# Kernel tuning notes

Measured on AMD Instinct MI355X. Metric: run time of the kernel, lower is better.

Reference implementation:

```python
import jax, jax.numpy as jnp
import numpy as np
import math

B, S, D = 2, 2048, 1024
H, HD = 16, 64
ROT = 16          # rotary_dim = head_dim * 0.25
FF = 4096
EPS = 1e-5


def setup_inputs() -> dict:
    key = jax.random.key(0)
    ks = jax.random.split(key, 12)
    sc = lambda *sh: 0.02
    inp = {
        "x": jax.random.normal(ks[0], (B, S, D), jnp.float32),
        "attention_mask": jnp.tril(jnp.ones((S, S), bool))[None, None],  # causal [1,1,S,S]
        "W_qkv": jax.random.normal(ks[1], (3 * D, D), jnp.float32) * 0.02,
        "b_qkv": jnp.zeros((3 * D,), jnp.float32),
        "W_o": jax.random.normal(ks[2], (D, D), jnp.float32) * 0.02,
        "b_o": jnp.zeros((D,), jnp.float32),
        "ln1_w": jnp.ones((D,), jnp.float32),
        "ln1_b": jnp.zeros((D,), jnp.float32),
        "ln2_w": jnp.ones((D,), jnp.float32),
        "ln2_b": jnp.zeros((D,), jnp.float32),
        "W1": jax.random.normal(ks[3], (FF, D), jnp.float32) * 0.02,
        "b1": jnp.zeros((FF,), jnp.float32),
        "W2": jax.random.normal(ks[4], (D, FF), jnp.float32) * 0.02,
        "b2": jnp.zeros((D,), jnp.float32),
    }
    # real rotary frequencies, shaped [1,1,S,ROT//2,2]
    inv_freq = 1.0 / (10000.0 ** (jnp.arange(0, ROT, 2, dtype=jnp.float32) / ROT))
    t = jnp.arange(S, dtype=jnp.float32)
    ang = t[:, None] * inv_freq[None, :]                      # [S, ROT//2]
    inp["freqs_cis"] = jnp.stack([jnp.cos(ang), jnp.sin(ang)], -1)[None, None]
    return inp


def layer_norm(x, w, b):
    mu = jnp.mean(x, -1, keepdims=True)
    var = jnp.mean(jnp.square(x - mu), -1, keepdims=True)
    return (x - mu) * jax.lax.rsqrt(var + EPS) * w + b


def apply_rotate_emb(x, freqs_cis):
    # x: [B,H,S,ROT]; freqs_cis: [1,1,S,ROT//2,2]
    x1, x2 = x[..., : ROT // 2], x[..., ROT // 2 :]
    cos, sin = freqs_cis[..., 0], freqs_cis[..., 1]
    return jnp.concatenate([x1 * cos - x2 * sin, x1 * sin + x2 * cos], -1)


def reference(x, attention_mask, freqs_cis, W_qkv, b_qkv, W_o, b_o,
              ln1_w, ln1_b, ln2_w, ln2_b, W1, b1, W2, b2):
    h = layer_norm(x, ln1_w, ln1_b)
    qkv = jnp.einsum("bsd,ed->bse", h, W_qkv) + b_qkv
    q, k, v = jnp.split(qkv, 3, axis=-1)
    to_heads = lambda t: t.reshape(B, S, H, HD).transpose(0, 2, 1, 3)  # [B,H,S,HD]
    q, k, v = to_heads(q), to_heads(k), to_heads(v)
    q = jnp.concatenate([apply_rotate_emb(q[..., :ROT], freqs_cis), q[..., ROT:]], -1)
    k = jnp.concatenate([apply_rotate_emb(k[..., :ROT], freqs_cis), k[..., ROT:]], -1)
    scores = jnp.einsum("bhqd,bhkd->bhqk", q, k) / math.sqrt(HD)
    scores = jnp.where(attention_mask, scores, -jnp.inf)
    probs = jax.nn.softmax(scores, axis=-1)
    out = jnp.einsum("bhqk,bhkd->bhqd", probs, v)
    out = out.transpose(0, 2, 1, 3).reshape(B, S, D)
    attn_out = jnp.einsum("bsd,ed->bse", out, W_o) + b_o
    # parallel residual (dropout is identity in eval)
    h2 = layer_norm(x, ln2_w, ln2_b)
    ff = jnp.einsum("bsf,df->bsd", jax.nn.gelu(jnp.einsum("bsd,fd->bsf", h2, W1) + b1, approximate=False), W2) + b2
    return x + ff + attn_out
```

## Files before the change

kernel.cpp:

```cpp
#include <hip/hip_runtime.h>

#define DEV __device__ __forceinline__

typedef __bf16 bf16;
typedef bf16 bf16x4 __attribute__((ext_vector_type(4)));
typedef bf16 bf16x8 __attribute__((ext_vector_type(8)));
typedef float f32x4 __attribute__((ext_vector_type(4)));

DEV f32x4 mfma16(bf16x8 a, bf16x8 b, f32x4 c) {
  return __builtin_amdgcn_mfma_f32_16x16x32_bf16(a, b, c, 0, 0, 0);
}

DEV void gload_lds16(const bf16* g, bf16* l) {
  __builtin_amdgcn_global_load_lds((const __attribute__((address_space(1))) void*)g,
                                   (__attribute__((address_space(3))) void*)l, 16, 0, 0);
}

#define PH_BAR __builtin_amdgcn_s_barrier()
#define VM(NSTR) asm volatile("s_waitcnt vmcnt(" NSTR ")" ::: "memory")
#define VMLG(NSTR) asm volatile("s_waitcnt vmcnt(" NSTR ") lgkmcnt(0)" ::: "memory")
#define WAITBAR(NSTR) asm volatile("s_waitcnt vmcnt(" NSTR ")\n\ts_barrier" ::: "memory")

DEV float fast_gelu(float x) {
  const float z = x * x;
  const float w = __builtin_fmaf(z, 0.1029353f, 2.3019853f);
  const float e = __builtin_amdgcn_exp2f(x * w);
  const float r = __builtin_amdgcn_rcpf(1.0f + e);
  return x - x * r;
}

__global__ __launch_bounds__(256) void ln_cast_all(
    const float* __restrict__ x,
    const float* __restrict__ ln1w, const float* __restrict__ ln1b,
    const float* __restrict__ ln2w, const float* __restrict__ ln2b,
    bf16* __restrict__ h1, bf16* __restrict__ h2,
    const float* __restrict__ Wqkv_f, const float* __restrict__ W1_f,
    const float* __restrict__ Wo_f, const float* __restrict__ W2_f,
    bf16* __restrict__ wQKV, bf16* __restrict__ w1, bf16* __restrict__ wCat)
{
  const int b = blockIdx.x, t = threadIdx.x;
  if (b < 4096) {
    __shared__ float red[2][4];
    const int lane = t & 63, wave = t >> 6;
    const float4 v = ((const float4*)(x + (size_t)b * 1024))[t];
    float vv[4] = {v.x, v.y, v.z, v.w};
    float s = vv[0] + vv[1] + vv[2] + vv[3];
    float q = vv[0]*vv[0] + vv[1]*vv[1] + vv[2]*vv[2] + vv[3]*vv[3];
    #pragma unroll
    for (int o = 32; o; o >>= 1) { s += __shfl_xor(s, o); q += __shfl_xor(q, o); }
    if (lane == 0) { red[0][wave] = s; red[1][wave] = q; }
    __syncthreads();
    s = red[0][0] + red[0][1] + red[0][2] + red[0][3];
    q = red[1][0] + red[1][1] + red[1][2] + red[1][3];
    const float mu = s * (1.0f / 1024.0f);
    const float var = q * (1.0f / 1024.0f) - mu * mu;
    const float rs = rsqrtf(var + 1e-5f);
    bf16x4 o1, o2;
    #pragma unroll
    for (int j = 0; j < 4; ++j) {
      const int i = t * 4 + j;
      const float xh = (vv[j] - mu) * rs;
      o1[j] = (bf16)(xh * ln1w[i] + ln1b[i]);
      o2[j] = (bf16)(xh * ln2w[i] + ln2b[i]);
    }
    *(bf16x4*)&h1[(size_t)b * 1024 + t * 4] = o1;
    *(bf16x4*)&h2[(size_t)b * 1024 + t * 4] = o2;
    return;
  }
  const int cb = b - 4096;
  if (cb < 3072) {
    const int i = cb * 256 + t;
    const float4 v = ((const float4*)Wqkv_f)[i];
    bf16x4 o = {(bf16)v.x, (bf16)v.y, (bf16)v.z, (bf16)v.w};
    ((bf16x4*)wQKV)[i] = o;
  } else if (cb < 7168) {
    const int i = (cb - 3072) * 256 + t;
    const float4 v = ((const float4*)W1_f)[i];
    bf16x4 o = {(bf16)v.x, (bf16)v.y, (bf16)v.z, (bf16)v.w};
    ((bf16x4*)w1)[i] = o;
  } else if (cb < 8192) {
    const int row = cb - 7168;
    const float4 v = *(const float4*)&Wo_f[(size_t)row * 1024 + t * 4];
    bf16x4 o = {(bf16)v.x, (bf16)v.y, (bf16)v.z, (bf16)v.w};
    *(bf16x4*)&wCat[(size_t)row * 5120 + t * 4] = o;
  } else {
    const int row = cb - 8192;
    #pragma unroll
    for (int k = 0; k < 4; ++k) {
      const int col = t * 4 + k * 1024;
      const float4 v = *(const float4*)&W2_f[(size_t)row * 4096 + col];
      bf16x4 o = {(bf16)v.x, (bf16)v.y, (bf16)v.z, (bf16)v.w};
      *(bf16x4*)&wCat[(size_t)row * 5120 + 1024 + col] = o;
    }
  }
}

DEV bf16x8 ldfrag(const bf16* unit, int lr, int g) {
  return *(const bf16x8*)&unit[lr * 32 + ((g ^ ((lr >> 1) & 3)) << 3)];
}
DEV void read_bfr(const bf16* unit, int blr, int g, bf16x8 bfr[4]) {
  #pragma unroll
  for (int nj = 0; nj < 4; ++nj) bfr[nj] = ldfrag(unit, blr + nj * 16, g);
}
DEV void read_af(const bf16* unit, int alr, int g, bf16x8 af[4]) {
  #pragma unroll
  for (int ml = 0; ml < 4; ++ml) af[ml] = ldfrag(unit, alr + ml * 16, g);
}
DEV void do_mfma(const bf16x8 af[4], const bf16x8 bfr[4], f32x4 acc[8][4], int mh) {
  __builtin_amdgcn_s_setprio(1);
  #pragma unroll
  for (int ml = 0; ml < 4; ++ml)
    #pragma unroll
    for (int nj = 0; nj < 4; ++nj)
      acc[mh * 4 + ml][nj] = mfma16(af[ml], bfr[nj], acc[mh * 4 + ml][nj]);
  __builtin_amdgcn_s_setprio(0);
}

DEV void gemm_kloop(bf16 (*As)[2][2][4096], bf16 (*Bs)[2][2][4096],
                    const bf16* aU[2][2], const bf16* bU[2][2],
                    int wave, int alr, int blr, int bub, int g, int nkt,
                    f32x4 acc[8][4])
{
  bf16x8 bfr[4], af[4];
#define STG_A(bf_, kkh_, ub_, ko_) gload_lds16(aU[kkh_][ub_] + (ko_), &As[bf_][kkh_][ub_][wave * 512])
#define STG_B(bf_, kkh_, ub_, ko_) gload_lds16(bU[kkh_][ub_] + (ko_), &Bs[bf_][kkh_][ub_][wave * 512])
  STG_B(0, 0, 0, 0); STG_B(0, 0, 1, 0); STG_A(0, 0, 0, 0); STG_A(0, 0, 1, 0);
  STG_B(0, 1, 0, 0); STG_B(0, 1, 1, 0); STG_A(0, 1, 0, 0); STG_A(0, 1, 1, 0);
  WAITBAR("4");

  for (int t = 0; t < nkt - 1; ++t) {
    const int buf = t & 1, nxt = buf ^ 1;
    const int ko = (t + 1) * 64;
    read_bfr(&Bs[buf][0][bub][0], blr, g, bfr);
    read_af(&As[buf][0][0][0], alr, g, af);
    STG_B(nxt, 0, 0, ko); STG_B(nxt, 0, 1, ko);
    do_mfma(af, bfr, acc, 0);
    read_af(&As[buf][0][1][0], alr, g, af);
    STG_A(nxt, 0, 0, ko); STG_A(nxt, 0, 1, ko);
    do_mfma(af, bfr, acc, 1);
    VMLG("4");
    PH_BAR;
    read_bfr(&Bs[buf][1][bub][0], blr, g, bfr);
    read_af(&As[buf][1][0][0], alr, g, af);
    STG_B(nxt, 1, 0, ko); STG_B(nxt, 1, 1, ko);
    do_mfma(af, bfr, acc, 0);
    read_af(&As[buf][1][1][0], alr, g, af);
    STG_A(nxt, 1, 0, ko); STG_A(nxt, 1, 1, ko);
    do_mfma(af, bfr, acc, 1);
    VMLG("4");
    PH_BAR;
  }
  {
    const int buf = (nkt - 1) & 1;
    read_bfr(&Bs[buf][0][bub][0], blr, g, bfr);
    read_af(&As[buf][0][0][0], alr, g, af);
    do_mfma(af, bfr, acc, 0);
    read_af(&As[buf][0][1][0], alr, g, af);
    do_mfma(af, bfr, acc, 1);
    VMLG("0");
    PH_BAR;
    read_bfr(&Bs[buf][1][bub][0], blr, g, bfr);
    read_af(&As[buf][1][0][0], alr, g, af);
    do_mfma(af, bfr, acc, 0);
    read_af(&As[buf][1][1][0], alr, g, af);
    do_mfma(af, bfr, acc, 1);
  }
#undef STG_A
#undef STG_B
}

template <int EPI>
__global__ __launch_bounds__(512) void gemm256(
    const bf16* __restrict__ A, const bf16* __restrict__ B,
    const float* __restrict__ bias, void* __restrict__ Cv,
    void* __restrict__ P1, void* __restrict__ P2, void* __restrict__ P3,
    const float* __restrict__ freqs,
    int K, int ldc, int ntiles, int nbx, int nkt)
{
  __shared__ __align__(16) bf16 As[2][2][2][4096];
  __shared__ __align__(16) bf16 Bs[2][2][2][4096];
  const int tid = threadIdx.x;
  const int lane = tid & 63, wave = tid >> 6;
  const int wm = wave >> 2, wn = wave & 3;
  const int g = lane >> 4, c = lane & 15;
  const int cpx = gridDim.x >> 3;
  const int swz = ((int)blockIdx.x & 7) * cpx + ((int)blockIdx.x >> 3);
  const int tile = swz % ntiles;
  const int sk = swz / ntiles;
  const int bm = (tile / nbx) * 256, bn = (tile % nbx) * 256;

  const int slr = tid >> 2;
  const int sch = (tid & 3) ^ ((tid >> 3) & 3);
  const bf16* aU[2][2];
  const bf16* bU[2][2];
  {
    const bf16* a0 = A + (size_t)(bm + ((slr >> 6) * 128) + (slr & 63)) * K
                       + (size_t)sk * nkt * 64 + sch * 8;
    const bf16* b0 = B + (size_t)(bn + slr) * K + (size_t)sk * nkt * 64 + sch * 8;
    aU[0][0] = a0;            aU[0][1] = a0 + (size_t)64 * K;
    aU[1][0] = a0 + 32;       aU[1][1] = a0 + (size_t)64 * K + 32;
    bU[0][0] = b0;            bU[0][1] = b0 + (size_t)128 * K;
    bU[1][0] = b0 + 32;       bU[1][1] = b0 + (size_t)128 * K + 32;
  }

  f32x4 acc[8][4] = {};
  const int alr = (wm << 6) + c;
  const int blr = ((wn & 1) << 6) + c;
  const int bub = wn >> 1;

  gemm_kloop(As, Bs, aU, bU, wave, alr, blr, bub, g, nkt, acc);

  const int row0 = bm + wm * 128 + 4 * g;
  const int col0 = bn + wn * 64 + c;

  if constexpr (EPI == 3) {
    bf16* Qb  = (bf16*)Cv;
    bf16* Kb  = (bf16*)P1;
    bf16* VTb = (bf16*)P2;
    const int which = bn >> 10;
    const int h = ((bn & 1023) >> 6) + wn;
    #pragma unroll
    for (int mi = 0; mi < 8; ++mi) {
      const int srow = row0 + mi * 16;
      const int bb = srow >> 11, sl0 = srow & 2047;
      #pragma unroll
      for (int nj = 0; nj < 4; ++nj) {
        const int d = nj * 16 + c;
        const float bv = bias[bn + wn * 64 + d];
        float vo[4];
        #pragma unroll
        for (int r = 0; r < 4; ++r) vo[r] = acc[mi][nj][r] + bv;
        if (which == 2) {
          bf16x4 o = {(bf16)vo[0], (bf16)vo[1], (bf16)vo[2], (bf16)vo[3]};
          *(bf16x4*)&VTb[((size_t)(bb * 16 + h) * 64 + d) * 2048 + sl0] = o;
        } else {
          if (nj == 0) {
            #pragma unroll
            for (int r = 0; r < 4; ++r) {
              const int sl = sl0 + r;
              const float cs = freqs[sl * 16 + (c & 7) * 2];
              const float sn = freqs[sl * 16 + (c & 7) * 2 + 1];
              const float p = __shfl_xor(vo[r], 8);
              vo[r] = (c < 8) ? (vo[r] * cs - p * sn) : (p * sn + vo[r] * cs);
            }
          }
          bf16* dst = (which == 0) ? Qb : Kb;
          const float sc = (which == 0) ? 0.18033688f  : 1.0f;
          #pragma unroll
          for (int r = 0; r < 4; ++r)
            dst[((size_t)(bb * 16 + h) * 2048 + (sl0 + r)) * 64 + d] = (bf16)(vo[r] * sc);
        }
      }
    }
    return;
  }

  bf16* Pp = nullptr;
  if constexpr (EPI == 2)
    Pp = (bf16*)((sk == 1) ? P1 : (sk == 2) ? P2 : (sk == 3) ? P3 : Cv);
  #pragma unroll
  for (int mi = 0; mi < 8; ++mi) {
    #pragma unroll
    for (int nj = 0; nj < 4; ++nj) {
      const int col = col0 + nj * 16;
      float bv = 0.0f;
      if constexpr (EPI < 2) bv = bias[col];
      #pragma unroll
      for (int r = 0; r < 4; ++r) {
        const size_t idx = (size_t)(row0 + mi * 16 + r) * ldc + col;
        float vo = acc[mi][nj][r] + bv;
        if constexpr (EPI == 0) {
          ((bf16*)Cv)[idx] = (bf16)vo;
        } else if constexpr (EPI == 1) {
          ((bf16*)Cv)[idx] = (bf16)fast_gelu(vo);
        } else {
          Pp[idx] = (bf16)vo;
        }
      }
    }
  }
}

__global__ __launch_bounds__(256) void combine_out(
    const bf16* __restrict__ q0, const bf16* __restrict__ q1,
    const bf16* __restrict__ q2, const bf16* __restrict__ q3,
    const float* __restrict__ x,
    const float* __restrict__ bo, const float* __restrict__ b2,
    float* __restrict__ out)
{
  const int row = blockIdx.x, t = threadIdx.x;
  const size_t base = (size_t)row * 1024 + t * 4;
  const bf16x4 a0 = *(const bf16x4*)&q0[base];
  const bf16x4 a1 = *(const bf16x4*)&q1[base];
  const bf16x4 a2 = *(const bf16x4*)&q2[base];
  const bf16x4 a3 = *(const bf16x4*)&q3[base];
  const float4 vx = *(const float4*)&x[base];
  const float4 vb = *(const float4*)&bo[t * 4];
  const float4 vc = *(const float4*)&b2[t * 4];
  float4 o;
  o.x = (float)a0[0] + (float)a1[0] + (float)a2[0] + (float)a3[0] + vx.x + vb.x + vc.x;
  o.y = (float)a0[1] + (float)a1[1] + (float)a2[1] + (float)a3[1] + vx.y + vb.y + vc.y;
  o.z = (float)a0[2] + (float)a1[2] + (float)a2[2] + (float)a3[2] + vx.z + vb.z + vc.z;
  o.w = (float)a0[3] + (float)a1[3] + (float)a2[3] + (float)a3[3] + vx.w + vb.w + vc.w;
  *(float4*)&out[base] = o;
}

__global__ __launch_bounds__(512, 4) void attn_kernel(
    const bf16* __restrict__ Q, const bf16* __restrict__ Kg,
    const bf16* __restrict__ VTg, bf16* __restrict__ O, int ldO)
{
  __shared__ __align__(16) bf16 Ks[4][64][64];
  __shared__ __align__(16) bf16 Vs[4][64][64];
  __shared__ __align__(16) bf16 Ps[8][16][64];

  const int tid = threadIdx.x;
  const int lane = tid & 63, wave = tid >> 6;
  const int g = lane >> 4, c = lane & 15;
  const int L = blockIdx.x;
  const int heavy = (L < 256);
  const int r = heavy ? L : (L - 256);
  const int bh = r >> 3;
  const int qtile = heavy ? (8 + (r & 7)) : (7 - (r & 7));
  const int qw = qtile * 128 + wave * 16;

  const bf16* Qp = Q + (size_t)bh * 2048 * 64;
  const bf16* Kp = Kg + (size_t)bh * 2048 * 64;
  const bf16* Vp = VTg + (size_t)bh * 64 * 2048;

  const int srow = lane >> 3;
  const int schunk = (lane & 7) ^ srow;
  const int svr = wave * 8 + srow;

  bf16x8 qreg[2];
  qreg[0] = *(const bf16x8*)&Qp[(size_t)(qw + c) * 64 + g * 8];
  qreg[1] = *(const bf16x8*)&Qp[(size_t)(qw + c) * 64 + 32 + g * 8];
  bf16x8 ones;
  #pragma unroll
  for (int j = 0; j < 8; ++j) ones[j] = (bf16)1.0f;

  const int cq = c & 7;
  int fo[4][2];
  #pragma unroll
  for (int i = 0; i < 4; ++i)
    #pragma unroll
    for (int kk = 0; kk < 2; ++kk)
      fo[i][kk] = (i * 16 + c) * 64 + (((kk * 4 + g) ^ cq) << 3);
  bf16* pw[4];
  #pragma unroll
  for (int kf = 0; kf < 4; ++kf)
    pw[kf] = &Ps[wave][c][((((kf * 2 + (g >> 1)) ^ cq) << 3)) + ((g & 1) << 2)];
  const bf16* pr[2];
  #pragma unroll
  for (int kk = 0; kk < 2; ++kk)
    pr[kk] = &Ps[wave][c][((kk * 4 + g) ^ cq) << 3];

  bf16* const kdst[4] = {&Ks[0][0][0] + wave * 512, &Ks[1][0][0] + wave * 512,
                         &Ks[2][0][0] + wave * 512, &Ks[3][0][0] + wave * 512};
  bf16* const vdst[4] = {&Vs[0][0][0] + wave * 512, &Vs[1][0][0] + wave * 512,
                         &Vs[2][0][0] + wave * 512, &Vs[3][0][0] + wave * 512};

  f32x4 oacc[4] = {};
  f32x4 lacc = {};
  float m_ = -1e30f;

  const int nkb = 2 * qtile + 2;
#define STAGE(j_, B4_) do {                                                         \
    gload_lds16(&Kp[(size_t)((j_) * 64 + svr) * 64 + schunk * 8], kdst[B4_]);       \
    gload_lds16(&Vp[(size_t)svr * 2048 + (j_) * 64 + schunk * 8], vdst[B4_]);       \
  } while (0)

  auto qkt = [&](f32x4* st, const bf16* kt) {
    __builtin_amdgcn_s_setprio(1);
    #pragma unroll
    for (int kf = 0; kf < 4; ++kf) {
      f32x4 z = {};
      z = mfma16(*(const bf16x8*)(kt + fo[kf][0]), qreg[0], z);
      st[kf] = mfma16(*(const bf16x8*)(kt + fo[kf][1]), qreg[1], z);
    }
    __builtin_amdgcn_s_setprio(0);
  };

  auto smpv = [&](const f32x4* st, int j_, const bf16* vt) {
    const int kbase = j_ * 64;
    float v[16];
    if (kbase + 63 > qw) {
      const int qrel = qw + c - kbase;
      #pragma unroll
      for (int kf = 0; kf < 4; ++kf)
        #pragma unroll
        for (int rr = 0; rr < 4; ++rr)
          v[kf * 4 + rr] = (kf * 16 + 4 * g + rr <= qrel) ? st[kf][rr] : -1e30f;
    } else {
      #pragma unroll
      for (int kf = 0; kf < 4; ++kf)
        #pragma unroll
        for (int rr = 0; rr < 4; ++rr)
          v[kf * 4 + rr] = st[kf][rr];
    }
    float u0 = fmaxf(fmaxf(v[0], v[1]), v[2]);
    float u1 = fmaxf(fmaxf(v[3], v[4]), v[5]);
    float u2 = fmaxf(fmaxf(v[6], v[7]), v[8]);
    float u3 = fmaxf(fmaxf(v[9], v[10]), v[11]);
    float u4 = fmaxf(fmaxf(v[12], v[13]), v[14]);
    float tm = fmaxf(fmaxf(fmaxf(u0, u1), u2), fmaxf(fmaxf(u3, u4), v[15]));
    if (__any(tm > m_ + 8.0f)) {
      float tr = fmaxf(tm, __shfl_xor(tm, 16));
      tr = fmaxf(tr, __shfl_xor(tr, 32));
      const float mn = fmaxf(m_, tr);
      const float alpha = __builtin_amdgcn_exp2f(m_ - mn);
      m_ = mn;
      lacc[0] *= alpha; lacc[1] *= alpha; lacc[2] *= alpha; lacc[3] *= alpha;
      #pragma unroll
      for (int df = 0; df < 4; ++df) {
        oacc[df][0] *= alpha; oacc[df][1] *= alpha;
        oacc[df][2] *= alpha; oacc[df][3] *= alpha;
      }
    }
    bf16 pq[16];
    #pragma unroll
    for (int i = 0; i < 16; ++i)
      pq[i] = (bf16)__builtin_amdgcn_exp2f(v[i] - m_);
    #pragma unroll
    for (int kf = 0; kf < 4; ++kf) {
      bf16x4 pk = {pq[kf * 4], pq[kf * 4 + 1], pq[kf * 4 + 2], pq[kf * 4 + 3]};
      *(bf16x4*)pw[kf] = pk;
    }
    bf16x8 pfrag0 = *(const bf16x8*)pr[0];
    bf16x8 pfrag1 = *(const bf16x8*)pr[1];
    __builtin_amdgcn_s_setprio(1);
    #pragma unroll
    for (int df = 0; df < 4; ++df) {
      oacc[df] = mfma16(*(const bf16x8*)(vt + fo[df][0]), pfrag0, oacc[df]);
      oacc[df] = mfma16(*(const bf16x8*)(vt + fo[df][1]), pfrag1, oacc[df]);
    }
    lacc = mfma16(ones, pfrag0, lacc);
    lacc = mfma16(ones, pfrag1, lacc);
    __builtin_amdgcn_s_setprio(0);
  };

#define ABODY(j_, BUF, stC, stN) do {                                          \
    const bool stg_ = ((j_) + 3 < nkb);                                        \
    if (stg_) STAGE((j_) + 3, (((BUF) + 3) & 3));                              \
    if (((j_) + 1) < nkb && ((j_) + 1) * 64 <= qw + 15)                        \
      qkt(stN, &Ks[((BUF) + 1) & 3][0][0]);                                    \
    if ((j_) * 64 <= qw + 15) smpv(stC, (j_), &Vs[(BUF)][0][0]);               \
    if (stg_) { VM("2"); } else { VM("0"); }                                   \
    PH_BAR;                                                                    \
  } while (0)

  f32x4 stA[4], stB[4];
  STAGE(0, 0); STAGE(1, 1); STAGE(2, 2);
  VM("2");
  PH_BAR;
  qkt(stA, &Ks[0][0][0]);

  const int nq = nkb >> 2;
  for (int qd = 0; qd < nq; ++qd) {
    const int j0 = 4 * qd;
    ABODY(j0 + 0, 0, stA, stB);
    ABODY(j0 + 1, 1, stB, stA);
    ABODY(j0 + 2, 2, stA, stB);
    ABODY(j0 + 3, 3, stB, stA);
  }
  if (nkb & 2) {
    ABODY(nkb - 2, 0, stA, stB);
    ABODY(nkb - 1, 1, stB, stA);
  }
#undef ABODY
#undef STAGE

  const int b = bh >> 4, h = bh & 15;
  const float inv = 1.0f / lacc[0];
  const int s = qw + c;
  #pragma unroll
  for (int df = 0; df < 4; ++df) {
    bf16x4 o;
    #pragma unroll
    for (int rr = 0; rr < 4; ++rr) o[rr] = (bf16)(oacc[df][rr] * inv);
    *(bf16x4*)&O[(size_t)(b * 2048 + s) * ldO + h * 64 + df * 16 + 4 * g] = o;
  }
}

extern "C" void kernel_launch(void* const* d_in, const int* in_sizes, int n_in,
                              void* d_out, int out_size, void* d_ws, size_t ws_size,
                              hipStream_t stream) {
  const float* x     = (const float*)d_in[0];
  const float* W_qkv = (const float*)d_in[2];
  const float* b_qkv = (const float*)d_in[3];
  const float* W_o   = (const float*)d_in[4];
  const float* b_o   = (const float*)d_in[5];
  const float* ln1w  = (const float*)d_in[6];
  const float* ln1b  = (const float*)d_in[7];
  const float* ln2w  = (const float*)d_in[8];
  const float* ln2b  = (const float*)d_in[9];
  const float* W1    = (const float*)d_in[10];
  const float* b1    = (const float*)d_in[11];
  const float* W2    = (const float*)d_in[12];
  const float* b2    = (const float*)d_in[13];
  const float* freqs = (const float*)d_in[14];
  float* out = (float*)d_out;

  char* ws = (char*)d_ws;
  const size_t MB = (size_t)1 << 20;
  bf16* h1   = (bf16*)(ws + 0 * MB);
  bf16* h2   = (bf16*)(ws + 8 * MB);
  bf16* wQKV = (bf16*)(ws + 16 * MB);
  bf16* wCat = (bf16*)(ws + 22 * MB);
  bf16* w1   = (bf16*)(ws + 32 * MB);
  bf16* Qb   = (bf16*)(ws + 64 * MB);
  bf16* Kb   = (bf16*)(ws + 72 * MB);
  bf16* VTb  = (bf16*)(ws + 80 * MB);
  bf16* A2   = (bf16*)(ws + 88 * MB);
  bf16* q0   = (bf16*)(ws + 0 * MB);
  bf16* q1   = (bf16*)(ws + 8 * MB);
  bf16* q2   = (bf16*)(ws + 40 * MB);
  bf16* q3   = (bf16*)(ws + 48 * MB);

  ln_cast_all<<<13312, 256, 0, stream>>>(x, ln1w, ln1b, ln2w, ln2b, h1, h2,
                                         W_qkv, W1, W_o, W2, wQKV, w1, wCat);
  gemm256<3><<<192, 512, 0, stream>>>(h1, wQKV, b_qkv, Qb,
                                      Kb, VTb, nullptr, freqs,
                                      1024, 3072, 192, 12, 16);
  attn_kernel<<<512, 512, 0, stream>>>(Qb, Kb, VTb, A2, 5120);
  gemm256<1><<<256, 512, 0, stream>>>(h2, w1, b1, A2 + 1024,
                                      nullptr, nullptr, nullptr, nullptr,
                                      1024, 5120, 256, 16, 16);
  gemm256<2><<<256, 512, 0, stream>>>(A2, wCat, nullptr, q0,
                                      q1, q2, q3, nullptr,
                                      5120, 1024, 64, 4, 20);
  combine_out<<<4096, 256, 0, stream>>>(q0, q1, q2, q3, x, b_o, b2, out);
}
```

Measured before the change: 184.7 us.

## Restructure GEMM k-loop to one barrier per tile with staggered half-step order

```diff
diff --git a/kernel.cpp b/kernel.cpp
--- a/kernel.cpp
+++ b/kernel.cpp
@@ -19,7 +19,6 @@
 #define PH_BAR __builtin_amdgcn_s_barrier()
 #define VM(NSTR) asm volatile("s_waitcnt vmcnt(" NSTR ")" ::: "memory")
 #define VMLG(NSTR) asm volatile("s_waitcnt vmcnt(" NSTR ") lgkmcnt(0)" ::: "memory")
-#define WAITBAR(NSTR) asm volatile("s_waitcnt vmcnt(" NSTR ")\n\ts_barrier" ::: "memory")
 
 DEV float fast_gelu(float x) {
   const float z = x * x;
@@ -115,56 +114,59 @@
       acc[mh * 4 + ml][nj] = mfma16(af[ml], bfr[nj], acc[mh * 4 + ml][nj]);
   __builtin_amdgcn_s_setprio(0);
 }
+DEV void half_step(const bf16* bunit, const bf16* aunit0, const bf16* aunit1,
+                   int alr, int blr, int g, f32x4 acc[8][4]) {
+  bf16x8 bfr[4], af[4];
+  read_bfr(bunit, blr, g, bfr);
+  read_af(aunit0, alr, g, af);
+  do_mfma(af, bfr, acc, 0);
+  read_af(aunit1, alr, g, af);
+  do_mfma(af, bfr, acc, 1);
+}
 
 DEV void gemm_kloop(bf16 (*As)[2][2][4096], bf16 (*Bs)[2][2][4096],
                     const bf16* aU[2][2], const bf16* bU[2][2],
-                    int wave, int alr, int blr, int bub, int g, int nkt,
+                    int wave, int wm, int alr, int blr, int bub, int g, int nkt,
                     f32x4 acc[8][4])
 {
-  bf16x8 bfr[4], af[4];
 #define STG_A(bf_, kkh_, ub_, ko_) gload_lds16(aU[kkh_][ub_] + (ko_), &As[bf_][kkh_][ub_][wave * 512])
 #define STG_B(bf_, kkh_, ub_, ko_) gload_lds16(bU[kkh_][ub_] + (ko_), &Bs[bf_][kkh_][ub_][wave * 512])
-  STG_B(0, 0, 0, 0); STG_B(0, 0, 1, 0); STG_A(0, 0, 0, 0); STG_A(0, 0, 1, 0);
-  STG_B(0, 1, 0, 0); STG_B(0, 1, 1, 0); STG_A(0, 1, 0, 0); STG_A(0, 1, 1, 0);
-  WAITBAR("4");
+#define STG_TILE(bf_, ko_) do {                                                   \
+    STG_B(bf_, 0, 0, ko_); STG_B(bf_, 0, 1, ko_);                                 \
+    STG_A(bf_, 0, 0, ko_); STG_A(bf_, 0, 1, ko_);                                 \
+    STG_B(bf_, 1, 0, ko_); STG_B(bf_, 1, 1, ko_);                                 \
+    STG_A(bf_, 1, 0, ko_); STG_A(bf_, 1, 1, ko_);                                 \
+  } while (0)
+
+  STG_TILE(0, 0);
+  VMLG("0");
+  PH_BAR;
 
   for (int t = 0; t < nkt - 1; ++t) {
     const int buf = t & 1, nxt = buf ^ 1;
     const int ko = (t + 1) * 64;
-    read_bfr(&Bs[buf][0][bub][0], blr, g, bfr);
-    read_af(&As[buf][0][0][0], alr, g, af);
-    STG_B(nxt, 0, 0, ko); STG_B(nxt, 0, 1, ko);
-    do_mfma(af, bfr, acc, 0);
-    read_af(&As[buf][0][1][0], alr, g, af);
-    STG_A(nxt, 0, 0, ko); STG_A(nxt, 0, 1, ko);
-    do_mfma(af, bfr, acc, 1);
-    VMLG("4");
-    PH_BAR;
-    read_bfr(&Bs[buf][1][bub][0], blr, g, bfr);
-    read_af(&As[buf][1][0][0], alr, g, af);
-    STG_B(nxt, 1, 0, ko); STG_B(nxt, 1, 1, ko);
-    do_mfma(af, bfr, acc, 0);
-    read_af(&As[buf][1][1][0], alr, g, af);
-    STG_A(nxt, 1, 0, ko); STG_A(nxt, 1, 1, ko);
-    do_mfma(af, bfr, acc, 1);
-    VMLG("4");
+    STG_TILE(nxt, ko);
+    if (wm == 0) {
+      half_step(&Bs[buf][0][bub][0], &As[buf][0][0][0], &As[buf][0][1][0], alr, blr, g, acc);
+      half_step(&Bs[buf][1][bub][0], &As[buf][1][0][0], &As[buf][1][1][0], alr, blr, g, acc);
+    } else {
+      half_step(&Bs[buf][1][bub][0], &As[buf][1][0][0], &As[buf][1][1][0], alr, blr, g, acc);
+      half_step(&Bs[buf][0][bub][0], &As[buf][0][0][0], &As[buf][0][1][0], alr, blr, g, acc);
+    }
+    VMLG("0");
     PH_BAR;
   }
   {
     const int buf = (nkt - 1) & 1;
-    read_bfr(&Bs[buf][0][bub][0], blr, g, bfr);
-    read_af(&As[buf][0][0][0], alr, g, af);
-    do_mfma(af, bfr, acc, 0);
-    read_af(&As[buf][0][1][0], alr, g, af);
-    do_mfma(af, bfr, acc, 1);
-    VMLG("0");
-    PH_BAR;
-    read_bfr(&Bs[buf][1][bub][0], blr, g, bfr);
-    read_af(&As[buf][1][0][0], alr, g, af);
-    do_mfma(af, bfr, acc, 0);
-    read_af(&As[buf][1][1][0], alr, g, af);
-    do_mfma(af, bfr, acc, 1);
-  }
+    if (wm == 0) {
+      half_step(&Bs[buf][0][bub][0], &As[buf][0][0][0], &As[buf][0][1][0], alr, blr, g, acc);
+      half_step(&Bs[buf][1][bub][0], &As[buf][1][0][0], &As[buf][1][1][0], alr, blr, g, acc);
+    } else {
+      half_step(&Bs[buf][1][bub][0], &As[buf][1][0][0], &As[buf][1][1][0], alr, blr, g, acc);
+      half_step(&Bs[buf][0][bub][0], &As[buf][0][0][0], &As[buf][0][1][0], alr, blr, g, acc);
+    }
+  }
+#undef STG_TILE
 #undef STG_A
 #undef STG_B
 }
@@ -208,7 +210,7 @@
   const int blr = ((wn & 1) << 6) + c;
   const int bub = wn >> 1;
 
-  gemm_kloop(As, Bs, aU, bU, wave, alr, blr, bub, g, nkt, acc);
+  gemm_kloop(As, Bs, aU, bU, wave, wm, alr, blr, bub, g, nkt, acc);
 
   const int row0 = bm + wm * 128 + 4 * g;
   const int col0 = bn + wn * 64 + c;
```

After: 204.8 us. +10.9%, slower.

## Pair heavy and light causal query tiles per block, two 16-row fragments per wave

Applied to the files above, without the earlier changes.

```diff
diff --git a/kernel.cpp b/kernel.cpp
--- a/kernel.cpp
+++ b/kernel.cpp
@@ -305,23 +305,22 @@
   *(float4*)&out[base] = o;
 }
 
-__global__ __launch_bounds__(512, 4) void attn_kernel(
+__global__ __launch_bounds__(512, 2) void attn_kernel(
     const bf16* __restrict__ Q, const bf16* __restrict__ Kg,
     const bf16* __restrict__ VTg, bf16* __restrict__ O, int ldO)
 {
   __shared__ __align__(16) bf16 Ks[4][64][64];
   __shared__ __align__(16) bf16 Vs[4][64][64];
-  __shared__ __align__(16) bf16 Ps[8][16][64];
+  __shared__ __align__(16) bf16 Ps[8][2][16][64];
 
   const int tid = threadIdx.x;
   const int lane = tid & 63, wave = tid >> 6;
   const int g = lane >> 4, c = lane & 15;
   const int L = blockIdx.x;
-  const int heavy = (L < 256);
-  const int r = heavy ? L : (L - 256);
-  const int bh = r >> 3;
-  const int qtile = heavy ? (8 + (r & 7)) : (7 - (r & 7));
-  const int qw = qtile * 128 + wave * 16;
+  const int bh = L >> 3, p = L & 7;
+  const int side = wave >> 2, ws = wave & 3;
+  const int qtile = side ? (7 - p) : (8 + p);
+  const int qw = qtile * 128 + ws * 32;
 
   const bf16* Qp = Q + (size_t)bh * 2048 * 64;
   const bf16* Kp = Kg + (size_t)bh * 2048 * 64;
@@ -331,9 +330,12 @@
   const int schunk = (lane & 7) ^ srow;
   const int svr = wave * 8 + srow;
 
-  bf16x8 qreg[2];
-  qreg[0] = *(const bf16x8*)&Qp[(size_t)(qw + c) * 64 + g * 8];
-  qreg[1] = *(const bf16x8*)&Qp[(size_t)(qw + c) * 64 + 32 + g * 8];
+  bf16x8 qreg[2][2];
+  #pragma unroll
+  for (int f = 0; f < 2; ++f) {
+    qreg[f][0] = *(const bf16x8*)&Qp[(size_t)(qw + f * 16 + c) * 64 + g * 8];
+    qreg[f][1] = *(const bf16x8*)&Qp[(size_t)(qw + f * 16 + c) * 64 + 32 + g * 8];
+  }
   bf16x8 ones;
   #pragma unroll
   for (int j = 0; j < 8; ++j) ones[j] = (bf16)1.0f;
@@ -345,110 +347,149 @@
     #pragma unroll
     for (int kk = 0; kk < 2; ++kk)
       fo[i][kk] = (i * 16 + c) * 64 + (((kk * 4 + g) ^ cq) << 3);
-  bf16* pw[4];
-  #pragma unroll
-  for (int kf = 0; kf < 4; ++kf)
-    pw[kf] = &Ps[wave][c][((((kf * 2 + (g >> 1)) ^ cq) << 3)) + ((g & 1) << 2)];
-  const bf16* pr[2];
-  #pragma unroll
-  for (int kk = 0; kk < 2; ++kk)
-    pr[kk] = &Ps[wave][c][((kk * 4 + g) ^ cq) << 3];
+  bf16* pw[2][4];
+  #pragma unroll
+  for (int f = 0; f < 2; ++f)
+    #pragma unroll
+    for (int kf = 0; kf < 4; ++kf)
+      pw[f][kf] = &Ps[wave][f][c][((((kf * 2 + (g >> 1)) ^ cq) << 3)) + ((g & 1) << 2)];
+  const bf16* pr[2][2];
+  #pragma unroll
+  for (int f = 0; f < 2; ++f)
+    #pragma unroll
+    for (int kk = 0; kk < 2; ++kk)
+      pr[f][kk] = &Ps[wave][f][c][((kk * 4 + g) ^ cq) << 3];
 
   bf16* const kdst[4] = {&Ks[0][0][0] + wave * 512, &Ks[1][0][0] + wave * 512,
                          &Ks[2][0][0] + wave * 512, &Ks[3][0][0] + wave * 512};
   bf16* const vdst[4] = {&Vs[0][0][0] + wave * 512, &Vs[1][0][0] + wave * 512,
                          &Vs[2][0][0] + wave * 512, &Vs[3][0][0] + wave * 512};
 
-  f32x4 oacc[4] = {};
-  f32x4 lacc = {};
-  float m_ = -1e30f;
-
-  const int nkb = 2 * qtile + 2;
+  f32x4 oacc[2][4] = {};
+  f32x4 lacc[2] = {};
+  float m0_ = -1e30f, m1_ = -1e30f;
+
+  const int nkb = 18 + 2 * p;
 #define STAGE(j_, B4_) do {                                                         \
     gload_lds16(&Kp[(size_t)((j_) * 64 + svr) * 64 + schunk * 8], kdst[B4_]);       \
     gload_lds16(&Vp[(size_t)svr * 2048 + (j_) * 64 + schunk * 8], vdst[B4_]);       \
   } while (0)
 
-  auto qkt = [&](f32x4* st, const bf16* kt) {
+  auto qkt = [&](f32x4 (*st)[4], const bf16* kt) {
     __builtin_amdgcn_s_setprio(1);
     #pragma unroll
     for (int kf = 0; kf < 4; ++kf) {
-      f32x4 z = {};
-      z = mfma16(*(const bf16x8*)(kt + fo[kf][0]), qreg[0], z);
-      st[kf] = mfma16(*(const bf16x8*)(kt + fo[kf][1]), qreg[1], z);
+      bf16x8 k0 = *(const bf16x8*)(kt + fo[kf][0]);
+      bf16x8 k1 = *(const bf16x8*)(kt + fo[kf][1]);
+      f32x4 z0 = {}, z1 = {};
+      z0 = mfma16(k0, qreg[0][0], z0);
+      st[0][kf] = mfma16(k1, qreg[0][1], z0);
+      z1 = mfma16(k0, qreg[1][0], z1);
+      st[1][kf] = mfma16(k1, qreg[1][1], z1);
     }
     __builtin_amdgcn_s_setprio(0);
   };
 
-  auto smpv = [&](const f32x4* st, int j_, const bf16* vt) {
+  auto smpv = [&](f32x4 (*st)[4], int j_, const bf16* vt) {
     const int kbase = j_ * 64;
-    float v[16];
+    float v0[16], v1[16];
     if (kbase + 63 > qw) {
-      const int qrel = qw + c - kbase;
+      const int qr0 = qw + c - kbase;
+      const int qr1 = qr0 + 16;
       #pragma unroll
       for (int kf = 0; kf < 4; ++kf)
         #pragma unroll
-        for (int rr = 0; rr < 4; ++rr)
-          v[kf * 4 + rr] = (kf * 16 + 4 * g + rr <= qrel) ? st[kf][rr] : -1e30f;
+        for (int rr = 0; rr < 4; ++rr) {
+          const int key = kf * 16 + 4 * g + rr;
+          v0[kf * 4 + rr] = (key <= qr0) ? st[0][kf][rr] : -1e30f;
+          v1[kf * 4 + rr] = (key <= qr1) ? st[1][kf][rr] : -1e30f;
+        }
     } else {
       #pragma unroll
       for (int kf = 0; kf < 4; ++kf)
         #pragma unroll
-        for (int rr = 0; rr < 4; ++rr)
-          v[kf * 4 + rr] = st[kf][rr];
-    }
-    float u0 = fmaxf(fmaxf(v[0], v[1]), v[2]);
-    float u1 = fmaxf(fmaxf(v[3], v[4]), v[5]);
-    float u2 = fmaxf(fmaxf(v[6], v[7]), v[8]);
-    float u3 = fmaxf(fmaxf(v[9], v[10]), v[11]);
-    float u4 = fmaxf(fmaxf(v[12], v[13]), v[14]);
-    float tm = fmaxf(fmaxf(fmaxf(u0, u1), u2), fmaxf(fmaxf(u3, u4), v[15]));
-    if (__any(tm > m_ + 8.0f)) {
-      float tr = fmaxf(tm, __shfl_xor(tm, 16));
-      tr = fmaxf(tr, __shfl_xor(tr, 32));
-      const float mn = fmaxf(m_, tr);
-      const float alpha = __builtin_amdgcn_exp2f(m_ - mn);
-      m_ = mn;
-      lacc[0] *= alpha; lacc[1] *= alpha; lacc[2] *= alpha; lacc[3] *= alpha;
+        for (int rr = 0; rr < 4; ++rr) {
+          v0[kf * 4 + rr] = st[0][kf][rr];
+          v1[kf * 4 + rr] = st[1][kf][rr];
+        }
+    }
+    float t0a = fmaxf(fmaxf(v0[0], v0[1]), v0[2]);
+    float t0b = fmaxf(fmaxf(v0[3], v0[4]), v0[5]);
+    float t0c = fmaxf(fmaxf(v0[6], v0[7]), v0[8]);
+    float t0d = fmaxf(fmaxf(v0[9], v0[10]), v0[11]);
+    float t0e = fmaxf(fmaxf(v0[12], v0[13]), v0[14]);
+    float tm0 = fmaxf(fmaxf(fmaxf(t0a, t0b), t0c), fmaxf(fmaxf(t0d, t0e), v0[15]));
+    float t1a = fmaxf(fmaxf(v1[0], v1[1]), v1[2]);
+    float t1b = fmaxf(fmaxf(v1[3], v1[4]), v1[5]);
+    float t1c = fmaxf(fmaxf(v1[6], v1[7]), v1[8]);
+    float t1d = fmaxf(fmaxf(v1[9], v1[10]), v1[11]);
+    float t1e = fmaxf(fmaxf(v1[12], v1[13]), v1[14]);
+    float tm1 = fmaxf(fmaxf(fmaxf(t1a, t1b), t1c), fmaxf(fmaxf(t1d, t1e), v1[15]));
+    if (__any(fmaxf(tm0 - m0_, tm1 - m1_) > 8.0f)) {
+      float tr0 = fmaxf(tm0, __shfl_xor(tm0, 16));
+      tr0 = fmaxf(tr0, __shfl_xor(tr0, 32));
+      float tr1 = fmaxf(tm1, __shfl_xor(tm1, 16));
+      tr1 = fmaxf(tr1, __shfl_xor(tr1, 32));
+      const float mn0 = fmaxf(m0_, tr0);
+      const float mn1 = fmaxf(m1_, tr1);
+      const float a0 = __builtin_amdgcn_exp2f(m0_ - mn0);
+      const float a1 = __builtin_amdgcn_exp2f(m1_ - mn1);
+      m0_ = mn0; m1_ = mn1;
+      lacc[0][0] *= a0; lacc[0][1] *= a0; lacc[0][2] *= a0; lacc[0][3] *= a0;
+      lacc[1][0] *= a1; lacc[1][1] *= a1; lacc[1][2] *= a1; lacc[1][3] *= a1;
       #pragma unroll
       for (int df = 0; df < 4; ++df) {
-        oacc[df][0] *= alpha; oacc[df][1] *= alpha;
-        oacc[df][2] *= alpha; oacc[df][3] *= alpha;
+        oacc[0][df][0] *= a0; oacc[0][df][1] *= a0;
+        oacc[0][df][2] *= a0; oacc[0][df][3] *= a0;
+        oacc[1][df][0] *= a1; oacc[1][df][1] *= a1;
+        oacc[1][df][2] *= a1; oacc[1][df][3] *= a1;
       }
     }
-    bf16 pq[16];
-    #pragma unroll
-    for (int i = 0; i < 16; ++i)
-      pq[i] = (bf16)__builtin_amdgcn_exp2f(v[i] - m_);
+    bf16 p0[16], p1[16];
+    #pragma unroll
+    for (int i = 0; i < 16; ++i) {
+      p0[i] = (bf16)__builtin_amdgcn_exp2f(v0[i] - m0_);
+      p1[i] = (bf16)__builtin_amdgcn_exp2f(v1[i] - m1_);
+    }
     #pragma unroll
     for (int kf = 0; kf < 4; ++kf) {
-      bf16x4 pk = {pq[kf * 4], pq[kf * 4 + 1], pq[kf * 4 + 2], pq[kf * 4 + 3]};
-      *(bf16x4*)pw[kf] = pk;
-    }
-    bf16x8 pfrag0 = *(const bf16x8*)pr[0];
-    bf16x8 pfrag1 = *(const bf16x8*)pr[1];
+      bf16x4 k0 = {p0[kf * 4], p0[kf * 4 + 1], p0[kf * 4 + 2], p0[kf * 4 + 3]};
+      bf16x4 k1 = {p1[kf * 4], p1[kf * 4 + 1], p1[kf * 4 + 2], p1[kf * 4 + 3]};
+      *(bf16x4*)pw[0][kf] = k0;
+      *(bf16x4*)pw[1][kf] = k1;
+    }
+    bf16x8 pf00 = *(const bf16x8*)pr[0][0];
+    bf16x8 pf01 = *(const bf16x8*)pr[0][1];
+    bf16x8 pf10 = *(const bf16x8*)pr[1][0];
+    bf16x8 pf11 = *(const bf16x8*)pr[1][1];
     __builtin_amdgcn_s_setprio(1);
     #pragma unroll
     for (int df = 0; df < 4; ++df) {
-      oacc[df] = mfma16(*(const bf16x8*)(vt + fo[df][0]), pfrag0, oacc[df]);
-      oacc[df] = mfma16(*(const bf16x8*)(vt + fo[df][1]), pfrag1, oacc[df]);
-    }
-    lacc = mfma16(ones, pfrag0, lacc);
-    lacc = mfma16(ones, pfrag1, lacc);
+      bf16x8 vv0 = *(const bf16x8*)(vt + fo[df][0]);
+      bf16x8 vv1 = *(const bf16x8*)(vt + fo[df][1]);
+      oacc[0][df] = mfma16(vv0, pf00, oacc[0][df]);
+      oacc[0][df] = mfma16(vv1, pf01, oacc[0][df]);
+      oacc[1][df] = mfma16(vv0, pf10, oacc[1][df]);
+      oacc[1][df] = mfma16(vv1, pf11, oacc[1][df]);
+    }
+    lacc[0] = mfma16(ones, pf00, lacc[0]);
+    lacc[0] = mfma16(ones, pf01, lacc[0]);
+    lacc[1] = mfma16(ones, pf10, lacc[1]);
+    lacc[1] = mfma16(ones, pf11, lacc[1]);
     __builtin_amdgcn_s_setprio(0);
   };
 
 #define ABODY(j_, BUF, stC, stN) do {                                          \
     const bool stg_ = ((j_) + 3 < nkb);                                        \
     if (stg_) STAGE((j_) + 3, (((BUF) + 3) & 3));                              \
-    if (((j_) + 1) < nkb && ((j_) + 1) * 64 <= qw + 15)                        \
+    if (((j_) + 1) < nkb && ((j_) + 1) * 64 <= qw + 31)                        \
       qkt(stN, &Ks[((BUF) + 1) & 3][0][0]);                                    \
-    if ((j_) * 64 <= qw + 15) smpv(stC, (j_), &Vs[(BUF)][0][0]);               \
+    if ((j_) * 64 <= qw + 31) smpv(stC, (j_), &Vs[(BUF)][0][0]);               \
     if (stg_) { VM("2"); } else { VM("0"); }                                   \
     PH_BAR;                                                                    \
   } while (0)
 
-  f32x4 stA[4], stB[4];
+  f32x4 stA[2][4], stB[2][4];
   STAGE(0, 0); STAGE(1, 1); STAGE(2, 2);
   VM("2");
   PH_BAR;
@@ -470,14 +511,17 @@
 #undef STAGE
 
   const int b = bh >> 4, h = bh & 15;
-  const float inv = 1.0f / lacc[0];
-  const int s = qw + c;
-  #pragma unroll
-  for (int df = 0; df < 4; ++df) {
-    bf16x4 o;
-    #pragma unroll
-    for (int rr = 0; rr < 4; ++rr) o[rr] = (bf16)(oacc[df][rr] * inv);
-    *(bf16x4*)&O[(size_t)(b * 2048 + s) * ldO + h * 64 + df * 16 + 4 * g] = o;
+  #pragma unroll
+  for (int f = 0; f < 2; ++f) {
+    const float inv = 1.0f / lacc[f][0];
+    const int s = qw + f * 16 + c;
+    #pragma unroll
+    for (int df = 0; df < 4; ++df) {
+      bf16x4 o;
+      #pragma unroll
+      for (int rr = 0; rr < 4; ++rr) o[rr] = (bf16)(oacc[f][df][rr] * inv);
+      *(bf16x4*)&O[(size_t)(b * 2048 + s) * ldO + h * 64 + df * 16 + 4 * g] = o;
+    }
   }
 }
 
@@ -521,7 +565,7 @@
   gemm256<3><<<192, 512, 0, stream>>>(h1, wQKV, b_qkv, Qb,
                                       Kb, VTb, nullptr, freqs,
                                       1024, 3072, 192, 12, 16);
-  attn_kernel<<<512, 512, 0, stream>>>(Qb, Kb, VTb, A2, 5120);
+  attn_kernel<<<256, 512, 0, stream>>>(Qb, Kb, VTb, A2, 5120);
   gemm256<1><<<256, 512, 0, stream>>>(h2, w1, b1, A2 + 1024,
                                       nullptr, nullptr, nullptr, nullptr,
                                       1024, 5120, 256, 16, 16);
```

After: 188.5 us. +2.1%, slower.
